# Optimization experiments

Measured on AMD Instinct MI355X. Metric: run time of the kernel, lower is better.

Reference implementation:

```python
import jax, jax.numpy as jnp
import numpy as np

B, S, H = 4, 2048, 576
NH, NKV, HD = 9, 3, 64  # num heads, kv heads, head_dim
ROPE_THETA = 100000.0
NEG = -1e9


def _rope_cos_sin(seq_len, dim, base, dtype):
    inv_freq = 1.0 / (base ** (jnp.arange(0, dim, 2, dtype=jnp.float32) / dim))
    t = jnp.arange(seq_len, dtype=jnp.float32)
    freqs = jnp.outer(t, inv_freq)            # [S, dim/2]
    emb = jnp.concatenate([freqs, freqs], -1)  # [S, dim]
    return jnp.cos(emb).astype(dtype), jnp.sin(emb).astype(dtype)


def _rotate_half(x):
    x1, x2 = x[..., : x.shape[-1] // 2], x[..., x.shape[-1] // 2 :]
    return jnp.concatenate([-x2, x1], axis=-1)


def setup_inputs() -> dict:
    key = jax.random.key(0)
    kx, kq, kk, kv, ko = jax.random.split(key, 5)
    x = jax.random.normal(kx, (B, S, H), dtype=jnp.float32)
    sc = 1.0 / np.sqrt(H)
    Wq = jax.random.normal(kq, (NH * HD, H), dtype=jnp.float32) * sc
    Wk = jax.random.normal(kk, (NKV * HD, H), dtype=jnp.float32) * sc
    Wv = jax.random.normal(kv, (NKV * HD, H), dtype=jnp.float32) * sc
    Wo = jax.random.normal(ko, (H, NH * HD), dtype=jnp.float32) * sc
    # additive causal mask [1,1,S,S]
    causal = jnp.tril(jnp.ones((S, S), dtype=bool))
    mask = jnp.where(causal, 0.0, NEG).astype(jnp.float32)[None, None]
    return {"x": x, "Wq": Wq, "Wk": Wk, "Wv": Wv, "Wo": Wo, "mask": mask}


def reference(x, Wq, Wk, Wv, Wo, mask):
    b, s, _ = x.shape
    q = (x @ Wq.T).reshape(b, s, NH, HD).transpose(0, 2, 1, 3)    # [b,nh,s,hd]
    k = (x @ Wk.T).reshape(b, s, NKV, HD).transpose(0, 2, 1, 3)   # [b,nkv,s,hd]
    v = (x @ Wv.T).reshape(b, s, NKV, HD).transpose(0, 2, 1, 3)
    cos, sin = _rope_cos_sin(s, HD, ROPE_THETA, x.dtype)          # [s,hd]
    cos, sin = cos[None, None], sin[None, None]
    q = q * cos + _rotate_half(q) * sin
    k = k * cos + _rotate_half(k) * sin
    groups = NH // NKV
    k = jnp.repeat(k, groups, axis=1)                              # [b,nh,s,hd]
    v = jnp.repeat(v, groups, axis=1)
    scores = jnp.einsum("bhqd,bhkd->bhqk", q, k) / np.sqrt(HD)
    scores = scores + mask
    attn = jax.nn.softmax(scores.astype(jnp.float32), axis=-1).astype(q.dtype)
    out = jnp.einsum("bhqk,bhkd->bhqd", attn, v)                   # [b,nh,s,hd]
    out = out.transpose(0, 2, 1, 3).reshape(b, s, NH * HD)
    return out @ Wo.T
```

## Files before the change

kernel.cpp:

```cpp
#include <hip/hip_runtime.h>
#include <hip/hip_bf16.h>
#include <cstdint>

typedef float  fvec4  __attribute__((ext_vector_type(4)));
typedef float  f32x4  __attribute__((ext_vector_type(4)));
typedef float  f32x16 __attribute__((ext_vector_type(16)));
typedef short  bvec8  __attribute__((ext_vector_type(8)));
typedef short  bvec4  __attribute__((ext_vector_type(4)));
typedef unsigned int uint;

#define B_    4
#define S_    2048
#define H_    576
#define NH_   9
#define NKV_  3
#define HD_   64
#define M_    8192
#define KVD_  192
#define NQKV_ 960

static __device__ __forceinline__ short f2bf(float f) {
  __hip_bfloat16 h = __float2bfloat16(f);
  short s;
  __builtin_memcpy(&s, &h, 2);
  return s;
}

static __device__ __forceinline__ uint pack2(float lo, float hi) {
  union { unsigned short u; __hip_bfloat16 h; } a, b;
  a.h = __float2bfloat16(lo);
  b.h = __float2bfloat16(hi);
  return (uint)a.u | ((uint)b.u << 16);
}

static __device__ __forceinline__ void gload16(void* lds, const void* g) {
  __builtin_amdgcn_global_load_lds((const __attribute__((address_space(1))) void*)g,
                                   (__attribute__((address_space(3))) void*)lds, 16, 0, 0);
}

__global__ __launch_bounds__(256) void rope_table_kernel(float* __restrict__ ct,
                                                         float* __restrict__ st) {
  int idx = blockIdx.x * 256 + threadIdx.x;
  int s = idx >> 5, i = idx & 31;
  float invf = powf(100000.0f, -(float)i / 32.0f);
  float fr = (float)s * invf;
  float sv, cv;
  sincosf(fr, &sv, &cv);
  ct[idx] = cv;
  st[idx] = sv;
}

__global__ __launch_bounds__(256) void convert_x_kernel(const float* __restrict__ in,
                                                        short* __restrict__ out, int n4) {
  int i = blockIdx.x * 256 + threadIdx.x;
  if (i >= n4) return;
  fvec4 v = *(const fvec4*)(in + (long)i * 4);
  bvec4 o;
  o[0] = f2bf(v[0]); o[1] = f2bf(v[1]); o[2] = f2bf(v[2]); o[3] = f2bf(v[3]);
  *(bvec4*)(out + (long)i * 4) = o;
}

__global__ __launch_bounds__(256) void convert_w_kernel(const float* __restrict__ wq,
                                                        const float* __restrict__ wk,
                                                        const float* __restrict__ wv,
                                                        const float* __restrict__ wo,
                                                        short* __restrict__ out) {
  long e = ((long)blockIdx.x * 256 + threadIdx.x) * 4;
  const float* src; long off;
  if (e < 331776)        { src = wq; off = e; }
  else if (e < 442368)   { src = wk; off = e - 331776; }
  else if (e < 552960)   { src = wv; off = e - 442368; }
  else                   { src = wo; off = e - 552960; }
  fvec4 v = *(const fvec4*)(src + off);
  bvec4 o;
  o[0] = f2bf(v[0]); o[1] = f2bf(v[1]); o[2] = f2bf(v[2]); o[3] = f2bf(v[3]);
  *(bvec4*)(out + e) = o;
}

#define GEMM_STAGE(buf, k0s)                                                   \
  do {                                                                         \
    short* asd = As + (buf) * 8192;                                            \
    short* wsd = Ws + (buf) * 4096;                                            \
    _Pragma("unroll")                                                          \
    for (int it = 0; it < 4; ++it) {                                           \
      int task = t + it * 256;                                                 \
      int r = task >> 3, c = task & 7;                                         \
      gload16(asd + ((t & 192) + it * 256) * 8,                                \
              A + (m0 + r) * (long)K + (k0s) + ((c ^ (r & 7)) << 3));          \
    }                                                                          \
    _Pragma("unroll")                                                          \
    for (int it = 0; it < 2; ++it) {                                           \
      int task = t + it * 256;                                                 \
      int r = task >> 3, c = task & 7;                                         \
      gload16(wsd + ((t & 192) + it * 256) * 8,                                \
              W + (n0 + r) * (long)K + (k0s) + ((c ^ (r & 7)) << 3));          \
    }                                                                          \
  } while (0)

__global__ __launch_bounds__(256) void gemm_mfma_kernel(const short* __restrict__ A,
                                                        const short* __restrict__ W,
                                                        float* __restrict__ C,
                                                        int M, int N, int K) {
  __shared__ __align__(16) short As[2 * 128 * 64];
  __shared__ __align__(16) short Ws[2 * 64 * 64];
  const int t = threadIdx.x;
  const int lane = t & 63;
  const int w = t >> 6;
  const int wm = w >> 1, wn = w & 1;
  const long m0 = (long)blockIdx.x * 128;
  const long n0 = (long)blockIdx.y * 64;
  const int lc = lane & 15, lg = lane >> 4;
  const int nk = K >> 6;

  f32x4 acc[4][2];
#pragma unroll
  for (int i = 0; i < 4; ++i)
#pragma unroll
    for (int j = 0; j < 2; ++j) acc[i][j] = (f32x4){0.f, 0.f, 0.f, 0.f};

  GEMM_STAGE(0, 0);
  asm volatile("s_waitcnt vmcnt(0)" ::: "memory");
  __builtin_amdgcn_s_barrier();

  for (int ks = 0; ks < nk; ++ks) {
    const int cur = ks & 1;
    if (ks + 1 < nk) GEMM_STAGE(1 - cur, (ks + 1) << 6);
    const short* as_ = As + cur * 8192;
    const short* ws_ = Ws + cur * 4096;
#pragma unroll
    for (int kk = 0; kk < 2; ++kk) {
      bvec8 af[4], bfr[2];
#pragma unroll
      for (int mt = 0; mt < 4; ++mt) {
        int r = wm * 64 + mt * 16 + lc;
        af[mt] = *(const bvec8*)(as_ + r * 64 + (((kk * 4 + lg) ^ (r & 7)) << 3));
      }
#pragma unroll
      for (int nt = 0; nt < 2; ++nt) {
        int r = wn * 32 + nt * 16 + lc;
        bfr[nt] = *(const bvec8*)(ws_ + r * 64 + (((kk * 4 + lg) ^ (r & 7)) << 3));
      }
#pragma unroll
      for (int mt = 0; mt < 4; ++mt)
#pragma unroll
        for (int nt = 0; nt < 2; ++nt)
          acc[mt][nt] = __builtin_amdgcn_mfma_f32_16x16x32_bf16(af[mt], bfr[nt],
                                                                acc[mt][nt], 0, 0, 0);
    }
    asm volatile("s_waitcnt vmcnt(0)" ::: "memory");
    __builtin_amdgcn_s_barrier();
  }

#pragma unroll
  for (int mt = 0; mt < 4; ++mt)
#pragma unroll
    for (int nt = 0; nt < 2; ++nt)
#pragma unroll
      for (int r = 0; r < 4; ++r) {
        long row = m0 + wm * 64 + mt * 16 + lg * 4 + r;
        long col = n0 + wn * 32 + nt * 16 + lc;
        C[row * (long)N + col] = acc[mt][nt][r];
      }
}

__global__ __launch_bounds__(256) void rope_convert_kernel(const float* __restrict__ qkv,
                                                           const float* __restrict__ ct,
                                                           const float* __restrict__ st,
                                                           short* __restrict__ qb,
                                                           short* __restrict__ kb) {
  const int QP = M_ * NH_ * 32;
  const int KP = M_ * NKV_ * 32;
  int idx = blockIdx.x * 256 + threadIdx.x;
  if (idx < QP) {
    int row = idx / (NH_ * 32);
    int rem = idx - row * (NH_ * 32);
    int h = rem >> 5, i = rem & 31;
    int s = row & (S_ - 1);
    float c = ct[s * 32 + i], sn = st[s * 32 + i];
    long base = (long)row * NQKV_ + h * HD_;
    float a = qkv[base + i], b2 = qkv[base + i + 32];
    long ob = (long)row * H_ + h * HD_;
    qb[ob + i]      = f2bf((a * c - b2 * sn) * 0.125f);
    qb[ob + i + 32] = f2bf((b2 * c + a * sn) * 0.125f);
  } else if (idx < QP + KP) {
    int j = idx - QP;
    int row = j / (NKV_ * 32);
    int rem = j - row * (NKV_ * 32);
    int h = rem >> 5, i = rem & 31;
    int s = row & (S_ - 1);
    float c = ct[s * 32 + i], sn = st[s * 32 + i];
    long base = (long)row * NQKV_ + 576 + h * HD_;
    float a = qkv[base + i], b2 = qkv[base + i + 32];
    long ob = (long)row * KVD_ + h * HD_;
    kb[ob + i]      = f2bf(a * c - b2 * sn);
    kb[ob + i + 32] = f2bf(b2 * c + a * sn);
  }
}

__global__ __launch_bounds__(256) void v_transpose_kernel(const float* __restrict__ qkv,
                                                          short* __restrict__ vt) {
  __shared__ float tile[64][65];
  const int t = threadIdx.x;
  const int rg = blockIdx.x;
  const int kvh = blockIdx.y;
  const int b = rg >> 5;
  const int s0 = (rg & 31) * 64;
#pragma unroll
  for (int it = 0; it < 4; ++it) {
    int r = (t >> 4) + it * 16;
    int c = (t & 15) * 4;
    fvec4 v = *(const fvec4*)(qkv + ((long)(b * S_ + s0 + r)) * NQKV_ + 768 + kvh * HD_ + c);
    tile[r][c] = v[0]; tile[r][c + 1] = v[1]; tile[r][c + 2] = v[2]; tile[r][c + 3] = v[3];
  }
  __syncthreads();
#pragma unroll
  for (int it = 0; it < 2; ++it) {
    int d = (t >> 3) + it * 32;
    int sl = (t & 7) * 8;
    bvec8 o;
#pragma unroll
    for (int j = 0; j < 8; ++j) o[j] = f2bf(tile[sl + j][d]);
    *(bvec8*)(vt + ((long)((b * NKV_ + kvh) * HD_ + d)) * S_ + s0 + sl) = o;
  }
}

#define ATTN_STAGE(buf, kb0s)                                                  \
  do {                                                                         \
    short* kd = Ks + (buf) * 4096;                                             \
    short* vd = Vs + (buf) * 4096;                                             \
    _Pragma("unroll")                                                          \
    for (int it = 0; it < 2; ++it) {                                           \
      int task = t + it * 256;                                                 \
      int r = task >> 3, c = task & 7;                                         \
      int db = ((t & 192) + it * 256) * 8;                                     \
      gload16(kd + db,                                                         \
              kb + ((long)(bS + (kb0s) + r)) * KVD_ + kvh * HD_ + ((c ^ (r & 7)) << 3)); \
      gload16(vd + db,                                                         \
              vt + (vbase + r) * S_ + (kb0s) + ((c ^ (r & 7)) << 3));          \
    }                                                                          \
  } while (0)

__global__ __launch_bounds__(256) void attn4w_kernel(const short* __restrict__ qb,
                                                     const short* __restrict__ kb,
                                                     const short* __restrict__ vt,
                                                     short* __restrict__ ao) {
  __shared__ __align__(16) short Ks[2 * 64 * 64];
  __shared__ __align__(16) short Vs[2 * 64 * 64];
  const int t  = threadIdx.x;
  const int w  = t >> 6;
  const int l  = t & 63;
  const int lq = l & 31;
  const int h2 = l >> 5;
  const int qt = 15 - (int)blockIdx.x;
  const int hq = blockIdx.y, b = blockIdx.z;
  const int kvh = hq / 3;
  const int q0 = qt * 128;
  const int q  = q0 + w * 32 + lq;
  const int nkv = 2 * qt + 2;
  const int bS = b * S_;
  const long vbase = (long)((b * NKV_ + kvh) * HD_);

  bvec8 qfr[4];
  {
    const short* qp = qb + ((long)(bS + q)) * H_ + hq * HD_ + h2 * 8;
#pragma unroll
    for (int c = 0; c < 4; ++c) qfr[c] = *(const bvec8*)(qp + c * 16);
  }

  f32x16 ot[2];
#pragma unroll
  for (int r = 0; r < 16; ++r) { ot[0][r] = 0.f; ot[1][r] = 0.f; }
  float m_run = -1e30f, l_run = 0.f;

  ATTN_STAGE(0, 0);
  asm volatile("s_waitcnt vmcnt(0)" ::: "memory");
  __builtin_amdgcn_s_barrier();

  for (int kv = 0; kv < nkv; ++kv) {
    const int cur = kv & 1;
    const int kb0 = kv * 64;
    if (kv + 1 < nkv) ATTN_STAGE(1 - cur, kb0 + 64);

    const short* ks_ = Ks + cur * 4096;
    const short* vs_ = Vs + cur * 4096;
    const bool active = (kb0 <= q0 + w * 32 + 31);
    if (active) {
      f32x16 sc[2];
#pragma unroll
      for (int r = 0; r < 16; ++r) { sc[0][r] = 0.f; sc[1][r] = 0.f; }
#pragma unroll
      for (int s = 0; s < 2; ++s) {
        int r = s * 32 + lq;
#pragma unroll
        for (int c = 0; c < 4; ++c) {
          bvec8 kf = *(const bvec8*)(ks_ + r * 64 + (((2 * c + h2) ^ (r & 7)) << 3));
          sc[s] = __builtin_amdgcn_mfma_f32_32x32x16_bf16(kf, qfr[c], sc[s], 0, 0, 0);
        }
      }
      if (kb0 + 63 > q0 + w * 32) {
#pragma unroll
        for (int s = 0; s < 2; ++s)
#pragma unroll
          for (int r = 0; r < 16; ++r) {
            int key = kb0 + s * 32 + (r & 3) + ((r >> 2) << 3) + h2 * 4;
            if (key > q) sc[s][r] = -1e30f;
          }
      }
      float mt = -1e30f;
#pragma unroll
      for (int s = 0; s < 2; ++s)
#pragma unroll
        for (int r = 0; r < 16; ++r) mt = fmaxf(mt, sc[s][r]);
      mt = fmaxf(mt, __shfl_xor(mt, 32));
      float mn = fmaxf(m_run, mt);
      float al = __expf(m_run - mn);
      float ps = 0.f;
#pragma unroll
      for (int s = 0; s < 2; ++s)
#pragma unroll
        for (int r = 0; r < 16; ++r) {
          float pv = __expf(sc[s][r] - mn);
          sc[s][r] = pv;
          ps += pv;
        }
      ps += __shfl_xor(ps, 32);
      l_run = l_run * al + ps;
      m_run = mn;
#pragma unroll
      for (int dt = 0; dt < 2; ++dt)
#pragma unroll
        for (int r = 0; r < 16; ++r) ot[dt][r] *= al;

      uint pa[2][4], pb[2][4];
#pragma unroll
      for (int s = 0; s < 2; ++s)
#pragma unroll
        for (int g = 0; g < 4; ++g) {
          pa[s][g] = pack2(sc[s][4 * g],     sc[s][4 * g + 1]);
          pb[s][g] = pack2(sc[s][4 * g + 2], sc[s][4 * g + 3]);
        }
      bvec8 pfr[4];
#pragma unroll
      for (int s = 0; s < 2; ++s)
#pragma unroll
        for (int kcp = 0; kcp < 2; ++kcp) {
          uint a0 = pa[s][2 * kcp],     b0 = pb[s][2 * kcp];
          uint a1 = pa[s][2 * kcp + 1], b1 = pb[s][2 * kcp + 1];
          uint ra0 = (uint)__shfl_xor((int)a0, 32);
          uint rb0 = (uint)__shfl_xor((int)b0, 32);
          uint ra1 = (uint)__shfl_xor((int)a1, 32);
          uint rb1 = (uint)__shfl_xor((int)b1, 32);
          union { uint u[4]; bvec8 v; } cvt;
          cvt.u[0] = h2 ? ra1 : a0;
          cvt.u[1] = h2 ? rb1 : b0;
          cvt.u[2] = h2 ? a1 : ra0;
          cvt.u[3] = h2 ? b1 : rb0;
          pfr[s * 2 + kcp] = cvt.v;
        }

#pragma unroll
      for (int dt = 0; dt < 2; ++dt) {
        int rv = dt * 32 + lq;
#pragma unroll
        for (int kc = 0; kc < 4; ++kc) {
          bvec8 vf_ = *(const bvec8*)(vs_ + rv * 64 + (((2 * kc + h2) ^ (rv & 7)) << 3));
          ot[dt] = __builtin_amdgcn_mfma_f32_32x32x16_bf16(vf_, pfr[kc], ot[dt], 0, 0, 0);
        }
      }
    }
    asm volatile("s_waitcnt vmcnt(0)" ::: "memory");
    __builtin_amdgcn_s_barrier();
  }

  const float inv = 1.0f / l_run;
  const long orow = (long)(bS + q);
#pragma unroll
  for (int dt = 0; dt < 2; ++dt)
#pragma unroll
    for (int g = 0; g < 4; ++g) {
      uint w0 = pack2(ot[dt][4 * g] * inv,     ot[dt][4 * g + 1] * inv);
      uint w1 = pack2(ot[dt][4 * g + 2] * inv, ot[dt][4 * g + 3] * inv);
      int d = dt * 32 + 8 * g + 4 * h2;
      uint2 stv; stv.x = w0; stv.y = w1;
      *(uint2*)(ao + orow * H_ + hq * HD_ + d) = stv;
    }
}

extern "C" void kernel_launch(void* const* d_in, const int* in_sizes, int n_in,
                              void* d_out, int out_size, void* d_ws, size_t ws_size,
                              hipStream_t stream) {
  const float* x  = (const float*)d_in[0];
  const float* Wq = (const float*)d_in[1];
  const float* Wk = (const float*)d_in[2];
  const float* Wv = (const float*)d_in[3];
  const float* Wo = (const float*)d_in[4];
  float* out = (float*)d_out;

  char* p = (char*)d_ws;
  float* ct   = (float*)p;  p += (long)S_ * 32 * 4;
  float* st   = (float*)p;  p += (long)S_ * 32 * 4;
  short* xb   = (short*)p;  p += (long)M_ * H_ * 2;
  short* w16  = (short*)p;  p += 884736L * 2;
  float* qkvf = (float*)p;  p += (long)M_ * NQKV_ * 4;
  short* qb   = (short*)p;  p += (long)M_ * H_ * 2;
  short* kb   = (short*)p;  p += (long)M_ * KVD_ * 2;

  short* vt = xb;
  short* ao = (short*)qkvf;
  short* wo16 = w16 + 552960;

  rope_table_kernel<<<256, 256, 0, stream>>>(ct, st);
  convert_x_kernel<<<(M_ * H_ / 4 + 255) / 256, 256, 0, stream>>>(x, xb, M_ * H_ / 4);
  convert_w_kernel<<<864, 256, 0, stream>>>(Wq, Wk, Wv, Wo, w16);

  gemm_mfma_kernel<<<dim3(64, 15), 256, 0, stream>>>(xb, w16, qkvf, M_, NQKV_, H_);

  rope_convert_kernel<<<12288, 256, 0, stream>>>(qkvf, ct, st, qb, kb);
  v_transpose_kernel<<<dim3(128, 3), 256, 0, stream>>>(qkvf, vt);

  attn4w_kernel<<<dim3(16, NH_, B_), 256, 0, stream>>>(qb, kb, vt, ao);

  gemm_mfma_kernel<<<dim3(64, 9), 256, 0, stream>>>(ao, wo16, out, M_, H_, H_);
}
```

Measured before the change: 228.3 us.

## Restructure GEMM/attention prefetch waits, use exp2 softmax with lazy rescale and packed bf16 converts

The GEMM and attention loops now prefetch the next tile and wait only for the previous tile's loads (partial vmcnt), using precomputed incremental source pointers instead of recomputing addresses on each stage. Softmax moves to base-2 exponentials by folding log2(e) into the Q scale, uses tree reductions for max and sum, and skips the running-max rescale unless the new max exceeds the old one by more than a threshold. Bf16 packing uses the hardware v_cvt_pk_bf16_f32 instruction. The lazy rescale could overflow if scores grow by more than the threshold, and the extra barrier per iteration adds synchronization.

```diff
diff --git a/kernel.cpp b/kernel.cpp
--- a/kernel.cpp
+++ b/kernel.cpp
@@ -26,11 +26,16 @@
   return s;
 }
 
-static __device__ __forceinline__ uint pack2(float lo, float hi) {
-  union { unsigned short u; __hip_bfloat16 h; } a, b;
-  a.h = __float2bfloat16(lo);
-  b.h = __float2bfloat16(hi);
-  return (uint)a.u | ((uint)b.u << 16);
+static __device__ __forceinline__ float fexp2(float x) {
+  float r;
+  asm("v_exp_f32 %0, %1" : "=v"(r) : "v"(x));
+  return r;
+}
+
+static __device__ __forceinline__ uint cvtpk(float lo, float hi) {
+  uint r;
+  asm("v_cvt_pk_bf16_f32 %0, %1, %2" : "=v"(r) : "v"(lo), "v"(hi));
+  return r;
 }
 
 static __device__ __forceinline__ void gload16(void* lds, const void* g) {
@@ -77,24 +82,17 @@
   *(bvec4*)(out + e) = o;
 }
 
-#define GEMM_STAGE(buf, k0s)                                                   \
+#define GEMM_STAGE(buf)                                                        \
   do {                                                                         \
     short* asd = As + (buf) * 8192;                                            \
     short* wsd = Ws + (buf) * 4096;                                            \
     _Pragma("unroll")                                                          \
-    for (int it = 0; it < 4; ++it) {                                           \
-      int task = t + it * 256;                                                 \
-      int r = task >> 3, c = task & 7;                                         \
-      gload16(asd + ((t & 192) + it * 256) * 8,                                \
-              A + (m0 + r) * (long)K + (k0s) + ((c ^ (r & 7)) << 3));          \
-    }                                                                          \
+    for (int it = 0; it < 4; ++it)                                             \
+      gload16(asd + dba + it * 2048, asrc + (long)32 * it * K);                \
     _Pragma("unroll")                                                          \
-    for (int it = 0; it < 2; ++it) {                                           \
-      int task = t + it * 256;                                                 \
-      int r = task >> 3, c = task & 7;                                         \
-      gload16(wsd + ((t & 192) + it * 256) * 8,                                \
-              W + (n0 + r) * (long)K + (k0s) + ((c ^ (r & 7)) << 3));          \
-    }                                                                          \
+    for (int it = 0; it < 2; ++it)                                             \
+      gload16(wsd + dba + it * 2048, wsrc + (long)32 * it * K);                \
+    asrc += 64; wsrc += 64;                                                    \
   } while (0)
 
 __global__ __launch_bounds__(256) void gemm_mfma_kernel(const short* __restrict__ A,
@@ -112,19 +110,29 @@
   const int lc = lane & 15, lg = lane >> 4;
   const int nk = K >> 6;
 
+  const int r0 = t >> 3, c0 = t & 7;
+  const short* asrc = A + (m0 + r0) * (long)K + ((c0 ^ (r0 & 7)) << 3);
+  const short* wsrc = W + (n0 + r0) * (long)K + ((c0 ^ (r0 & 7)) << 3);
+  const int dba = (t & 192) * 8;
+
   f32x4 acc[4][2];
 #pragma unroll
   for (int i = 0; i < 4; ++i)
 #pragma unroll
     for (int j = 0; j < 2; ++j) acc[i][j] = (f32x4){0.f, 0.f, 0.f, 0.f};
 
-  GEMM_STAGE(0, 0);
-  asm volatile("s_waitcnt vmcnt(0)" ::: "memory");
-  __builtin_amdgcn_s_barrier();
+  GEMM_STAGE(0);
 
   for (int ks = 0; ks < nk; ++ks) {
     const int cur = ks & 1;
-    if (ks + 1 < nk) GEMM_STAGE(1 - cur, (ks + 1) << 6);
+    __builtin_amdgcn_s_barrier();
+    if (ks + 1 < nk) {
+      GEMM_STAGE(1 - cur);
+      asm volatile("s_waitcnt vmcnt(6)" ::: "memory");
+    } else {
+      asm volatile("s_waitcnt vmcnt(0)" ::: "memory");
+    }
+    __builtin_amdgcn_s_barrier();
     const short* as_ = As + cur * 8192;
     const short* ws_ = Ws + cur * 4096;
 #pragma unroll
@@ -147,8 +155,6 @@
           acc[mt][nt] = __builtin_amdgcn_mfma_f32_16x16x32_bf16(af[mt], bfr[nt],
                                                                 acc[mt][nt], 0, 0, 0);
     }
-    asm volatile("s_waitcnt vmcnt(0)" ::: "memory");
-    __builtin_amdgcn_s_barrier();
   }
 
 #pragma unroll
@@ -170,6 +176,7 @@
                                                            short* __restrict__ kb) {
   const int QP = M_ * NH_ * 32;
   const int KP = M_ * NKV_ * 32;
+  const float QSC = 0.18033688011112042f;
   int idx = blockIdx.x * 256 + threadIdx.x;
   if (idx < QP) {
     int row = idx / (NH_ * 32);
@@ -180,8 +187,8 @@
     long base = (long)row * NQKV_ + h * HD_;
     float a = qkv[base + i], b2 = qkv[base + i + 32];
     long ob = (long)row * H_ + h * HD_;
-    qb[ob + i]      = f2bf((a * c - b2 * sn) * 0.125f);
-    qb[ob + i + 32] = f2bf((b2 * c + a * sn) * 0.125f);
+    qb[ob + i]      = f2bf((a * c - b2 * sn) * QSC);
+    qb[ob + i + 32] = f2bf((b2 * c + a * sn) * QSC);
   } else if (idx < QP + KP) {
     int j = idx - QP;
     int row = j / (NKV_ * 32);
@@ -224,20 +231,15 @@
   }
 }
 
-#define ATTN_STAGE(buf, kb0s)                                                  \
+#define ATTN_STAGE(buf)                                                        \
   do {                                                                         \
     short* kd = Ks + (buf) * 4096;                                             \
     short* vd = Vs + (buf) * 4096;                                             \
-    _Pragma("unroll")                                                          \
-    for (int it = 0; it < 2; ++it) {                                           \
-      int task = t + it * 256;                                                 \
-      int r = task >> 3, c = task & 7;                                         \
-      int db = ((t & 192) + it * 256) * 8;                                     \
-      gload16(kd + db,                                                         \
-              kb + ((long)(bS + (kb0s) + r)) * KVD_ + kvh * HD_ + ((c ^ (r & 7)) << 3)); \
-      gload16(vd + db,                                                         \
-              vt + (vbase + r) * S_ + (kb0s) + ((c ^ (r & 7)) << 3));          \
-    }                                                                          \
+    gload16(kd + db0, ksrc);                                                   \
+    gload16(kd + db1, ksrc + 32 * KVD_);                                       \
+    gload16(vd + db0, vsrc);                                                   \
+    gload16(vd + db1, (const short*)vsrc + (long)32 * S_);                     \
+    ksrc += 64 * KVD_;  vsrc += 64;                                            \
   } while (0)
 
 __global__ __launch_bounds__(256) void attn4w_kernel(const short* __restrict__ qb,
@@ -260,6 +262,12 @@
   const int bS = b * S_;
   const long vbase = (long)((b * NKV_ + kvh) * HD_);
 
+  const int r0 = t >> 3, c0 = t & 7;
+  const int sw0 = (c0 ^ (r0 & 7)) << 3;
+  const short* ksrc = kb + ((long)(bS + r0)) * KVD_ + kvh * HD_ + sw0;
+  const short* vsrc = vt + (vbase + r0) * S_ + sw0;
+  const int db0 = (t & 192) * 8, db1 = ((t & 192) + 256) * 8;
+
   bvec8 qfr[4];
   {
     const short* qp = qb + ((long)(bS + q)) * H_ + hq * HD_ + h2 * 8;
@@ -272,19 +280,23 @@
   for (int r = 0; r < 16; ++r) { ot[0][r] = 0.f; ot[1][r] = 0.f; }
   float m_run = -1e30f, l_run = 0.f;
 
-  ATTN_STAGE(0, 0);
-  asm volatile("s_waitcnt vmcnt(0)" ::: "memory");
-  __builtin_amdgcn_s_barrier();
+  ATTN_STAGE(0);
 
   for (int kv = 0; kv < nkv; ++kv) {
     const int cur = kv & 1;
     const int kb0 = kv * 64;
-    if (kv + 1 < nkv) ATTN_STAGE(1 - cur, kb0 + 64);
+    __builtin_amdgcn_s_barrier();
+    if (kv + 1 < nkv) {
+      ATTN_STAGE(1 - cur);
+      asm volatile("s_waitcnt vmcnt(4)" ::: "memory");
+    } else {
+      asm volatile("s_waitcnt vmcnt(0)" ::: "memory");
+    }
+    __builtin_amdgcn_s_barrier();
 
     const short* ks_ = Ks + cur * 4096;
     const short* vs_ = Vs + cur * 4096;
-    const bool active = (kb0 <= q0 + w * 32 + 31);
-    if (active) {
+    if (kb0 <= q0 + w * 32 + 31) {
       f32x16 sc[2];
 #pragma unroll
       for (int r = 0; r < 16; ++r) { sc[0][r] = 0.f; sc[1][r] = 0.f; }
@@ -306,38 +318,44 @@
             if (key > q) sc[s][r] = -1e30f;
           }
       }
-      float mt = -1e30f;
+      float red[16];
+#pragma unroll
+      for (int i = 0; i < 16; ++i) red[i] = fmaxf(sc[0][i], sc[1][i]);
+#pragma unroll
+      for (int off = 8; off >= 1; off >>= 1)
+#pragma unroll
+        for (int i = 0; i < off; ++i) red[i] = fmaxf(red[i], red[i + off]);
+      float mt = fmaxf(red[0], __shfl_xor(red[0], 32));
+      if (!__all(mt <= m_run + 8.0f)) {
+        float mn = fmaxf(m_run, mt);
+        float al = fexp2(m_run - mn);
+        l_run *= al;
+#pragma unroll
+        for (int dt = 0; dt < 2; ++dt)
+#pragma unroll
+          for (int r = 0; r < 16; ++r) ot[dt][r] *= al;
+        m_run = mn;
+      }
 #pragma unroll
       for (int s = 0; s < 2; ++s)
 #pragma unroll
-        for (int r = 0; r < 16; ++r) mt = fmaxf(mt, sc[s][r]);
-      mt = fmaxf(mt, __shfl_xor(mt, 32));
-      float mn = fmaxf(m_run, mt);
-      float al = __expf(m_run - mn);
-      float ps = 0.f;
+        for (int r = 0; r < 16; ++r) sc[s][r] = fexp2(sc[s][r] - m_run);
+      float sr[16];
+#pragma unroll
+      for (int i = 0; i < 16; ++i) sr[i] = sc[0][i] + sc[1][i];
+#pragma unroll
+      for (int off = 8; off >= 1; off >>= 1)
+#pragma unroll
+        for (int i = 0; i < off; ++i) sr[i] += sr[i + off];
+      l_run += sr[0] + __shfl_xor(sr[0], 32);
+
+      uint pa[2][4], pb[2][4];
 #pragma unroll
       for (int s = 0; s < 2; ++s)
 #pragma unroll
-        for (int r = 0; r < 16; ++r) {
-          float pv = __expf(sc[s][r] - mn);
-          sc[s][r] = pv;
-          ps += pv;
-        }
-      ps += __shfl_xor(ps, 32);
-      l_run = l_run * al + ps;
-      m_run = mn;
-#pragma unroll
-      for (int dt = 0; dt < 2; ++dt)
-#pragma unroll
-        for (int r = 0; r < 16; ++r) ot[dt][r] *= al;
-
-      uint pa[2][4], pb[2][4];
-#pragma unroll
-      for (int s = 0; s < 2; ++s)
-#pragma unroll
         for (int g = 0; g < 4; ++g) {
-          pa[s][g] = pack2(sc[s][4 * g],     sc[s][4 * g + 1]);
-          pb[s][g] = pack2(sc[s][4 * g + 2], sc[s][4 * g + 3]);
+          pa[s][g] = cvtpk(sc[s][4 * g],     sc[s][4 * g + 1]);
+          pb[s][g] = cvtpk(sc[s][4 * g + 2], sc[s][4 * g + 3]);
         }
       bvec8 pfr[4];
 #pragma unroll
@@ -368,8 +386,6 @@
         }
       }
     }
-    asm volatile("s_waitcnt vmcnt(0)" ::: "memory");
-    __builtin_amdgcn_s_barrier();
   }
 
   const float inv = 1.0f / l_run;
@@ -378,8 +394,8 @@
   for (int dt = 0; dt < 2; ++dt)
 #pragma unroll
     for (int g = 0; g < 4; ++g) {
-      uint w0 = pack2(ot[dt][4 * g] * inv,     ot[dt][4 * g + 1] * inv);
-      uint w1 = pack2(ot[dt][4 * g + 2] * inv, ot[dt][4 * g + 3] * inv);
+      uint w0 = cvtpk(ot[dt][4 * g] * inv,     ot[dt][4 * g + 1] * inv);
+      uint w1 = cvtpk(ot[dt][4 * g + 2] * inv, ot[dt][4 * g + 3] * inv);
       int d = dt * 32 + 8 * g + 4 * h2;
       uint2 stv; stv.x = w0; stv.y = w1;
       *(uint2*)(ao + orow * H_ + hq * HD_ + d) = stv;
```

Measured after the change: 215.8 us. 1.06x faster.
